# Kernel tuning notes

Hardware: AMD Instinct MI355X
Metric: run time of the kernel (lower is better)

Reference implementation:

```python
import jax, jax.numpy as jnp
import numpy as np

N_NODES = 100000
N_EDGES = 1000000
D_IN = 64
D_OUT = 64


def setup_inputs() -> dict:
    key = jax.random.key(0)
    k_x, k_e, k_w, k_b = jax.random.split(key, 4)
    x = jax.random.normal(k_x, (N_NODES, D_IN), dtype=jnp.float32)
    edge_index = jax.random.randint(k_e, (2, N_EDGES), 0, N_NODES, dtype=jnp.int64)
    # degrees of destination nodes (what the caller is expected to supply);
    # clamp to >=1 to avoid division by zero for isolated nodes
    deg = jax.ops.segment_sum(jnp.ones((N_EDGES,), jnp.float32), edge_index[1], num_segments=N_NODES)
    node_degrees = jnp.maximum(deg, 1.0)
    W = jax.random.normal(k_w, (D_OUT, D_IN), dtype=jnp.float32) * (1.0 / np.sqrt(D_IN))
    b = jax.random.normal(k_b, (D_OUT,), dtype=jnp.float32) * 0.01
    return {"x": x, "edge_index": edge_index, "node_degrees": node_degrees, "W": W, "b": b}


def reference(x, edge_index, node_degrees, W, b):
    # Original does argsort+cumsum+boundary segment-sum; mathematically this is
    # a scatter-add of gathered neighbor features into dst, i.e. a segment sum.
    src, dst = edge_index[0], edge_index[1]
    agg = jax.ops.segment_sum(x[src], dst, num_segments=x.shape[0])  # [N, D_IN]
    mean = agg / node_degrees[:, None]
    return mean @ W.T + b  # [N, D_OUT]
```

## Files before the change

### kernel.cpp

```cpp
#include <hip/hip_runtime.h>


#define D 64
#define BSHIFT 7
#define BNODES (1 << BSHIFT)
#define CAP 2048
#define GTHREADS 512
#define PERTHREAD (CAP / GTHREADS)
#define MAXB 2048

__device__ inline int detect_stride_block(const unsigned* __restrict__ words,
                                          int E, int* sflag) {
    int t = threadIdx.x;
    if (t < 64) {
        unsigned v = (t < E) ? words[2 * t + 1] : 0u;
        int any = __any(v != 0u);
        if (t == 0) *sflag = any ? 1 : 2;
    }
    __syncthreads();
    return *sflag;
}

__device__ inline unsigned pack_bf16(float a, float b) {
    unsigned ua = __float_as_uint(a), ub = __float_as_uint(b);
    ua += 0x7fffu + ((ua >> 16) & 1u);
    ub += 0x7fffu + ((ub >> 16) & 1u);
    return (ua >> 16) | (ub & 0xffff0000u);
}

__global__ __launch_bounds__(256) void deg_bucket_hist(
        const float* __restrict__ deg, int* __restrict__ bcnt, int N, int nb) {
    __shared__ int lh[8];
    int t = threadIdx.x;
    if (t < 8) lh[t] = 0;
    __syncthreads();
    int n0 = blockIdx.x * 1024 + t * 4;
    int v = 0;
    #pragma unroll
    for (int j = 0; j < 4; ++j) { int n = n0 + j; if (n < N) v += (int)(deg[n] + 0.5f); }
    atomicAdd(&lh[t >> 5], v);
    __syncthreads();
    if (t < 8) {
        int b = blockIdx.x * 8 + t;
        if (b < nb) bcnt[b] = lh[t];
    }
}

__global__ __launch_bounds__(256) void bucket_scan(
        const int* __restrict__ bcnt, int* __restrict__ offs,
        int* __restrict__ cursor, int nb) {
    __shared__ int s[256];
    int t = threadIdx.x;
    int c[8]; int v = 0;
    #pragma unroll
    for (int j = 0; j < 8; ++j) {
        int i = t * 8 + j;
        c[j] = (i < nb) ? bcnt[i] : 0;
        v += c[j];
    }
    int own = v;
    s[t] = v;
    __syncthreads();
    for (int off = 1; off < 256; off <<= 1) {
        int u = (t >= off) ? s[t - off] : 0;
        __syncthreads();
        s[t] += u;
        __syncthreads();
    }
    int run = s[t] - own;
    #pragma unroll
    for (int j = 0; j < 8; ++j) {
        int i = t * 8 + j;
        if (i < nb) { offs[i] = run; cursor[i] = run; run += c[j]; }
    }
}

__global__ __launch_bounds__(256) void partition_kernel(
        const unsigned* __restrict__ ewords, int* __restrict__ cursor,
        unsigned* __restrict__ pairs, int E, int nb) {
    __shared__ int sflag;
    __shared__ int lhist[MAXB];
    __shared__ int lbase[MAXB];
    int s = detect_stride_block(ewords, E, &sflag);
    int t = threadIdx.x;
    for (int sub = 0; sub < 2; ++sub) {
        int base = blockIdx.x * 8192 + sub * 4096;
        if (base >= E) break;
        for (int i = t; i < nb; i += 256) lhist[i] = 0;
        __syncthreads();
        unsigned pv[16]; int bk[16];
        #pragma unroll
        for (int k = 0; k < 16; ++k) {
            int e = base + k * 256 + t;
            bk[k] = -1;
            if (e < E) {
                unsigned src = ewords[(size_t)e * s];
                unsigned dst = ewords[((size_t)E + e) * s];
                bk[k] = (int)(dst >> BSHIFT);
                pv[k] = src | ((dst & (BNODES - 1)) << 17);
                atomicAdd(&lhist[bk[k]], 1);
            }
        }
        __syncthreads();
        for (int hb = t; hb < nb; hb += 256) {
            int cc = lhist[hb];
            if (cc) lbase[hb] = atomicAdd(&cursor[hb], cc);
            lhist[hb] = 0;
        }
        __syncthreads();
        #pragma unroll
        for (int k = 0; k < 16; ++k) {
            if (bk[k] >= 0) {
                int lpos = atomicAdd(&lhist[bk[k]], 1);
                pairs[lbase[bk[k]] + lpos] = pv[k];
            }
        }
        __syncthreads();
    }
}

__global__ __launch_bounds__(256, 4) void xw_kernel(
        const float* __restrict__ x, const float* __restrict__ W,
        unsigned* __restrict__ y2, int N) {
    __shared__ float Wt[64 * 68];
    __shared__ float xs[64 * 68];
    int t = threadIdx.x;
    for (int i = t; i < 64 * 64; i += 256) {
        int o = i >> 6, k = i & 63;
        Wt[k * 68 + o] = W[i];
    }
    int base = blockIdx.x * 64;
    int row = t >> 4, c4 = (t & 15) * 4;
    #pragma unroll
    for (int r = 0; r < 4; ++r) {
        int nl = row + r * 16;
        int n = base + nl;
        float4 v = {0.f, 0.f, 0.f, 0.f};
        if (n < N) v = *(const float4*)(x + (size_t)n * 64 + c4);
        *(float4*)&xs[nl * 68 + c4] = v;
    }
    __syncthreads();
    int o4 = (t & 15) * 4, nl4 = (t >> 4) * 4;
    float acc[4][4];
    #pragma unroll
    for (int i = 0; i < 4; ++i)
        #pragma unroll
        for (int j = 0; j < 4; ++j) acc[i][j] = 0.f;
    #pragma unroll 2
    for (int k0 = 0; k0 < 64; k0 += 4) {
        float a[4][4], wv[4][4];
        #pragma unroll
        for (int i = 0; i < 4; ++i)
            *(float4*)a[i] = *(const float4*)&xs[(nl4 + i) * 68 + k0];
        #pragma unroll
        for (int dk = 0; dk < 4; ++dk)
            *(float4*)wv[dk] = *(const float4*)&Wt[(k0 + dk) * 68 + o4];
        #pragma unroll
        for (int i = 0; i < 4; ++i)
            #pragma unroll
            for (int j = 0; j < 4; ++j)
                acc[i][j] += a[i][0] * wv[0][j] + a[i][1] * wv[1][j]
                           + a[i][2] * wv[2][j] + a[i][3] * wv[3][j];
    }
    int n0 = base + nl4;
    #pragma unroll
    for (int i = 0; i < 4; ++i) {
        if (n0 + i < N) {
            uint2 p;
            p.x = pack_bf16(acc[i][0], acc[i][1]);
            p.y = pack_bf16(acc[i][2], acc[i][3]);
            *(uint2*)(y2 + (size_t)(n0 + i) * 32 + (o4 >> 1)) = p;
        }
    }
}

__global__ __launch_bounds__(GTHREADS) void bucket_gather(
        const unsigned* __restrict__ y2, const unsigned* __restrict__ pairs,
        const int* __restrict__ offs, const int* __restrict__ endc,
        const float* __restrict__ deg, const float* __restrict__ b,
        float* __restrict__ out, int N) {
    __shared__ unsigned list[CAP];
    __shared__ int cnt[BNODES], st[BNODES], sc[BNODES];
    int t = threadIdx.x;
    int bkt = blockIdx.x, base = bkt << BSHIFT;
    int start = offs[bkt], end = endc[bkt];
    int lane = t & 63, w = t >> 6;
    int g = lane >> 4, c = lane & 15;
    float4 bv = ((const float4*)b)[c];
    int nchunk = (end - start + CAP - 1) / CAP;
    if (nchunk < 1) nchunk = 1;

    for (int ci = 0; ci < nchunk; ++ci) {
        int e0 = start + ci * CAP;
        int cn = end - e0; if (cn > CAP) cn = CAP; if (cn < 0) cn = 0;
        if (t < BNODES) cnt[t] = 0;
        __syncthreads();
        unsigned pv[PERTHREAD];
        #pragma unroll
        for (int j = 0; j < PERTHREAD; ++j) {
            int i = t + j * GTHREADS;
            pv[j] = (i < cn) ? pairs[e0 + i] : 0xFFFFFFFFu;
            if (i < cn) atomicAdd(&cnt[pv[j] >> 17], 1);
        }
        __syncthreads();
        if (t < BNODES) sc[t] = cnt[t];
        __syncthreads();
        for (int off = 1; off < BNODES; off <<= 1) {
            int v = (t < BNODES && t >= off) ? sc[t - off] : 0;
            __syncthreads();
            if (t < BNODES) sc[t] += v;
            __syncthreads();
        }
        if (t < BNODES) { st[t] = sc[t] - cnt[t]; sc[t] = sc[t] - cnt[t]; }
        __syncthreads();
        #pragma unroll
        for (int j = 0; j < PERTHREAD; ++j) {
            if (pv[j] != 0xFFFFFFFFu) {
                int pos = atomicAdd(&sc[pv[j] >> 17], 1);
                list[pos] = pv[j] & 0x1FFFFu;
            }
        }
        __syncthreads();

        for (int nl0 = w * 16; nl0 < w * 16 + 16; nl0 += 4) {
            int mynode = nl0 + g;
            int n = base + mynode;
            int s0 = st[mynode], e1 = s0 + cnt[mynode];
            float ax = 0.f, ay = 0.f, az = 0.f, aw = 0.f;
            for (int i = s0; i < e1; ++i) {
                unsigned src = list[i];
                uint2 u = *(const uint2*)(y2 + (size_t)src * 32 + c * 2);
                ax += __uint_as_float(u.x << 16);
                ay += __uint_as_float(u.x & 0xffff0000u);
                az += __uint_as_float(u.y << 16);
                aw += __uint_as_float(u.y & 0xffff0000u);
            }
            if (n < N) {
                float* op = out + (size_t)n * 64 + c * 4;
                if (nchunk == 1) {
                    float invd = 1.0f / deg[n];
                    float4 o4 = {ax * invd + bv.x, ay * invd + bv.y,
                                 az * invd + bv.z, aw * invd + bv.w};
                    *(float4*)op = o4;
                } else {
                    float4 p = {0.f, 0.f, 0.f, 0.f};
                    if (ci > 0) p = *(const float4*)op;
                    p.x += ax; p.y += ay; p.z += az; p.w += aw;
                    if (ci == nchunk - 1) {
                        float invd = 1.0f / deg[n];
                        p = {p.x * invd + bv.x, p.y * invd + bv.y,
                             p.z * invd + bv.z, p.w * invd + bv.w};
                    }
                    *(float4*)op = p;
                }
            }
        }
        __syncthreads();
    }
}

__global__ __launch_bounds__(256) void scatter_kernel(
        const float* __restrict__ x, const unsigned* __restrict__ ewords,
        float* __restrict__ agg, int E) {
    __shared__ int sflag;
    int s = detect_stride_block(ewords, E, &sflag);
    int gid = blockIdx.x * blockDim.x + threadIdx.x;
    int e = gid >> 4, q = gid & 15;
    if (e >= E) return;
    int src = (int)ewords[(size_t)e * s];
    int dst = (int)ewords[((size_t)E + e) * s];
    const float4 v = *(const float4*)(x + (size_t)src * D + q * 4);
    float* p = agg + (size_t)dst * D + q * 4;
    unsafeAtomicAdd(p + 0, v.x);
    unsafeAtomicAdd(p + 1, v.y);
    unsafeAtomicAdd(p + 2, v.z);
    unsafeAtomicAdd(p + 3, v.w);
}

__global__ __launch_bounds__(256) void gemm_kernel(
        float* __restrict__ inout, const float* __restrict__ deg,
        const float* __restrict__ W, const float* __restrict__ b, int nNodes) {
    __shared__ float Wt[64 * 65];
    __shared__ float rows[4 * 64];
    int t = threadIdx.x;
    for (int i = t; i < 64 * 64; i += 256) {
        int o = i >> 6, k = i & 63;
        Wt[k * 65 + o] = W[i];
    }
    int base = blockIdx.x * 4;
    int nl = t >> 6, o = t & 63;
    int n = base + nl;
    if (n < nNodes) {
        float invd = 1.0f / deg[n];
        rows[nl * 64 + o] = inout[(size_t)n * 64 + o] * invd;
    }
    __syncthreads();
    if (n >= nNodes) return;
    float acc = b[o];
    #pragma unroll
    for (int k = 0; k < 64; ++k)
        acc += rows[nl * 64 + k] * Wt[k * 65 + o];
    inout[(size_t)n * 64 + o] = acc;
}

extern "C" void kernel_launch(void* const* d_in, const int* in_sizes, int n_in,
                              void* d_out, int out_size, void* d_ws, size_t ws_size,
                              hipStream_t stream) {
    const float*    x      = (const float*)d_in[0];
    const unsigned* ewords = (const unsigned*)d_in[1];
    const float*    deg    = (const float*)d_in[2];
    const float*    W      = (const float*)d_in[3];
    const float*    b      = (const float*)d_in[4];
    float*          out    = (float*)d_out;

    const int E = in_sizes[1] / 2;
    const int N = in_sizes[2];
    const int nb = (N + BNODES - 1) >> BSHIFT;

    char* ws = (char*)d_ws;
    size_t bcntB = MAXB * 4, offB = MAXB * 4, curB = MAXB * 4;
    size_t pairB = (((size_t)E + N) * 4 + 63) & ~63ull;
    size_t need  = bcntB + offB + curB + pairB + (size_t)N * 32 * 4;

    if (ws_size >= need && N < (1 << 17) && nb <= MAXB) {
        int*      bcnt   = (int*)ws;
        int*      offs   = (int*)(ws + bcntB);
        int*      cursor = (int*)(ws + bcntB + offB);
        unsigned* pairs  = (unsigned*)(ws + bcntB + offB + curB);
        unsigned* y2     = (unsigned*)(ws + bcntB + offB + curB + pairB);

        deg_bucket_hist<<<(N + 1023) / 1024, 256, 0, stream>>>(deg, bcnt, N, nb);
        bucket_scan<<<1, 256, 0, stream>>>(bcnt, offs, cursor, nb);
        partition_kernel<<<(E + 8191) / 8192, 256, 0, stream>>>(
            ewords, cursor, pairs, E, nb);
        xw_kernel<<<(N + 63) / 64, 256, 0, stream>>>(x, W, y2, N);
        bucket_gather<<<nb, GTHREADS, 0, stream>>>(
            y2, pairs, offs, cursor, deg, b, out, N);
    } else {
        hipMemsetAsync(d_out, 0, (size_t)out_size * sizeof(float), stream);
        long long sthreads = (long long)E * 16;
        int sblocks = (int)((sthreads + 255) / 256);
        scatter_kernel<<<sblocks, 256, 0, stream>>>(x, ewords, out, E);
        gemm_kernel<<<(N + 3) / 4, 256, 0, stream>>>(out, deg, W, b, N);
    }
}
```

Measured before the change: 161.6 us.

## Use fixed-capacity edge buckets with spill and fuse partition with XW GEMM

```diff
diff --git a/kernel.cpp b/kernel.cpp
--- a/kernel.cpp
+++ b/kernel.cpp
@@ -28,234 +28,189 @@
     return (ua >> 16) | (ub & 0xffff0000u);
 }
 
-__global__ __launch_bounds__(256) void deg_bucket_hist(
-        const float* __restrict__ deg, int* __restrict__ bcnt, int N, int nb) {
-    __shared__ int lh[8];
+__global__ __launch_bounds__(256, 4) void partition_xw_kernel(
+        const unsigned* __restrict__ ewords, int* __restrict__ cursor,
+        unsigned* __restrict__ pairs, uint2* __restrict__ spill,
+        int* __restrict__ spillCnt,
+        const float* __restrict__ x, const float* __restrict__ W,
+        unsigned* __restrict__ y2, int E, int N, int nb, int pblocks) {
+    __shared__ __align__(16) char smem[34832];
     int t = threadIdx.x;
-    if (t < 8) lh[t] = 0;
-    __syncthreads();
-    int n0 = blockIdx.x * 1024 + t * 4;
-    int v = 0;
-    #pragma unroll
-    for (int j = 0; j < 4; ++j) { int n = n0 + j; if (n < N) v += (int)(deg[n] + 0.5f); }
-    atomicAdd(&lh[t >> 5], v);
-    __syncthreads();
-    if (t < 8) {
-        int b = blockIdx.x * 8 + t;
-        if (b < nb) bcnt[b] = lh[t];
-    }
-}
-
-__global__ __launch_bounds__(256) void bucket_scan(
-        const int* __restrict__ bcnt, int* __restrict__ offs,
-        int* __restrict__ cursor, int nb) {
-    __shared__ int s[256];
-    int t = threadIdx.x;
-    int c[8]; int v = 0;
-    #pragma unroll
-    for (int j = 0; j < 8; ++j) {
-        int i = t * 8 + j;
-        c[j] = (i < nb) ? bcnt[i] : 0;
-        v += c[j];
-    }
-    int own = v;
-    s[t] = v;
-    __syncthreads();
-    for (int off = 1; off < 256; off <<= 1) {
-        int u = (t >= off) ? s[t - off] : 0;
+
+    if ((int)blockIdx.x < pblocks) {
+        int* lhist = (int*)smem;
+        int* lbase = lhist + MAXB;
+        int* sflag = lbase + MAXB;
+        int s = detect_stride_block(ewords, E, sflag);
+        for (int sub = 0; sub < 2; ++sub) {
+            int base = blockIdx.x * 8192 + sub * 4096;
+            if (base >= E) break;
+            for (int i = t; i < nb; i += 256) lhist[i] = 0;
+            __syncthreads();
+            unsigned pv[16]; int bk[16];
+            #pragma unroll
+            for (int k = 0; k < 16; ++k) {
+                int e = base + k * 256 + t;
+                bk[k] = -1;
+                if (e < E) {
+                    unsigned src = ewords[(size_t)e * s];
+                    unsigned dst = ewords[((size_t)E + e) * s];
+                    bk[k] = (int)(dst >> BSHIFT);
+                    pv[k] = src | ((dst & (BNODES - 1)) << 17);
+                    atomicAdd(&lhist[bk[k]], 1);
+                }
+            }
+            __syncthreads();
+            for (int hb = t; hb < nb; hb += 256) {
+                int cc = lhist[hb];
+                if (cc) lbase[hb] = atomicAdd(&cursor[hb], cc);
+                lhist[hb] = 0;
+            }
+            __syncthreads();
+            #pragma unroll
+            for (int k = 0; k < 16; ++k) {
+                if (bk[k] >= 0) {
+                    int lpos = lbase[bk[k]] + atomicAdd(&lhist[bk[k]], 1);
+                    if (lpos < CAP) {
+                        pairs[(size_t)bk[k] * CAP + lpos] = pv[k];
+                    } else {
+                        int si = atomicAdd(spillCnt, 1);
+                        unsigned dst = ((unsigned)bk[k] << BSHIFT) | (pv[k] >> 17);
+                        spill[si] = make_uint2(pv[k] & 0x1FFFFu, dst);
+                    }
+                }
+            }
+            __syncthreads();
+        }
+    } else {
+        float* Wt = (float*)smem;
+        float* xs = Wt + 64 * 68;
+        for (int i = t; i < 64 * 64; i += 256) {
+            int o = i >> 6, k = i & 63;
+            Wt[k * 68 + o] = W[i];
+        }
+        int base = ((int)blockIdx.x - pblocks) * 64;
+        int row = t >> 4, c4 = (t & 15) * 4;
+        #pragma unroll
+        for (int r = 0; r < 4; ++r) {
+            int nl = row + r * 16;
+            int n = base + nl;
+            float4 v = {0.f, 0.f, 0.f, 0.f};
+            if (n < N) v = *(const float4*)(x + (size_t)n * 64 + c4);
+            *(float4*)&xs[nl * 68 + c4] = v;
+        }
         __syncthreads();
-        s[t] += u;
-        __syncthreads();
-    }
-    int run = s[t] - own;
-    #pragma unroll
-    for (int j = 0; j < 8; ++j) {
-        int i = t * 8 + j;
-        if (i < nb) { offs[i] = run; cursor[i] = run; run += c[j]; }
-    }
-}
-
-__global__ __launch_bounds__(256) void partition_kernel(
-        const unsigned* __restrict__ ewords, int* __restrict__ cursor,
-        unsigned* __restrict__ pairs, int E, int nb) {
-    __shared__ int sflag;
-    __shared__ int lhist[MAXB];
-    __shared__ int lbase[MAXB];
-    int s = detect_stride_block(ewords, E, &sflag);
-    int t = threadIdx.x;
-    for (int sub = 0; sub < 2; ++sub) {
-        int base = blockIdx.x * 8192 + sub * 4096;
-        if (base >= E) break;
-        for (int i = t; i < nb; i += 256) lhist[i] = 0;
-        __syncthreads();
-        unsigned pv[16]; int bk[16];
-        #pragma unroll
-        for (int k = 0; k < 16; ++k) {
-            int e = base + k * 256 + t;
-            bk[k] = -1;
-            if (e < E) {
-                unsigned src = ewords[(size_t)e * s];
-                unsigned dst = ewords[((size_t)E + e) * s];
-                bk[k] = (int)(dst >> BSHIFT);
-                pv[k] = src | ((dst & (BNODES - 1)) << 17);
-                atomicAdd(&lhist[bk[k]], 1);
-            }
-        }
-        __syncthreads();
-        for (int hb = t; hb < nb; hb += 256) {
-            int cc = lhist[hb];
-            if (cc) lbase[hb] = atomicAdd(&cursor[hb], cc);
-            lhist[hb] = 0;
-        }
-        __syncthreads();
-        #pragma unroll
-        for (int k = 0; k < 16; ++k) {
-            if (bk[k] >= 0) {
-                int lpos = atomicAdd(&lhist[bk[k]], 1);
-                pairs[lbase[bk[k]] + lpos] = pv[k];
-            }
-        }
-        __syncthreads();
-    }
-}
-
-__global__ __launch_bounds__(256, 4) void xw_kernel(
-        const float* __restrict__ x, const float* __restrict__ W,
-        unsigned* __restrict__ y2, int N) {
-    __shared__ float Wt[64 * 68];
-    __shared__ float xs[64 * 68];
-    int t = threadIdx.x;
-    for (int i = t; i < 64 * 64; i += 256) {
-        int o = i >> 6, k = i & 63;
-        Wt[k * 68 + o] = W[i];
-    }
-    int base = blockIdx.x * 64;
-    int row = t >> 4, c4 = (t & 15) * 4;
-    #pragma unroll
-    for (int r = 0; r < 4; ++r) {
-        int nl = row + r * 16;
-        int n = base + nl;
-        float4 v = {0.f, 0.f, 0.f, 0.f};
-        if (n < N) v = *(const float4*)(x + (size_t)n * 64 + c4);
-        *(float4*)&xs[nl * 68 + c4] = v;
-    }
-    __syncthreads();
-    int o4 = (t & 15) * 4, nl4 = (t >> 4) * 4;
-    float acc[4][4];
-    #pragma unroll
-    for (int i = 0; i < 4; ++i)
-        #pragma unroll
-        for (int j = 0; j < 4; ++j) acc[i][j] = 0.f;
-    #pragma unroll 2
-    for (int k0 = 0; k0 < 64; k0 += 4) {
-        float a[4][4], wv[4][4];
+        int o4 = (t & 15) * 4, nl4 = (t >> 4) * 4;
+        float acc[4][4];
         #pragma unroll
         for (int i = 0; i < 4; ++i)
-            *(float4*)a[i] = *(const float4*)&xs[(nl4 + i) * 68 + k0];
+            #pragma unroll
+            for (int j = 0; j < 4; ++j) acc[i][j] = 0.f;
+        #pragma unroll 2
+        for (int k0 = 0; k0 < 64; k0 += 4) {
+            float a[4][4], wv[4][4];
+            #pragma unroll
+            for (int i = 0; i < 4; ++i)
+                *(float4*)a[i] = *(const float4*)&xs[(nl4 + i) * 68 + k0];
+            #pragma unroll
+            for (int dk = 0; dk < 4; ++dk)
+                *(float4*)wv[dk] = *(const float4*)&Wt[(k0 + dk) * 68 + o4];
+            #pragma unroll
+            for (int i = 0; i < 4; ++i)
+                #pragma unroll
+                for (int j = 0; j < 4; ++j)
+                    acc[i][j] += a[i][0] * wv[0][j] + a[i][1] * wv[1][j]
+                               + a[i][2] * wv[2][j] + a[i][3] * wv[3][j];
+        }
+        int n0 = base + nl4;
         #pragma unroll
-        for (int dk = 0; dk < 4; ++dk)
-            *(float4*)wv[dk] = *(const float4*)&Wt[(k0 + dk) * 68 + o4];
-        #pragma unroll
-        for (int i = 0; i < 4; ++i)
-            #pragma unroll
-            for (int j = 0; j < 4; ++j)
-                acc[i][j] += a[i][0] * wv[0][j] + a[i][1] * wv[1][j]
-                           + a[i][2] * wv[2][j] + a[i][3] * wv[3][j];
-    }
-    int n0 = base + nl4;
-    #pragma unroll
-    for (int i = 0; i < 4; ++i) {
-        if (n0 + i < N) {
-            uint2 p;
-            p.x = pack_bf16(acc[i][0], acc[i][1]);
-            p.y = pack_bf16(acc[i][2], acc[i][3]);
-            *(uint2*)(y2 + (size_t)(n0 + i) * 32 + (o4 >> 1)) = p;
+        for (int i = 0; i < 4; ++i) {
+            if (n0 + i < N) {
+                uint2 p;
+                p.x = pack_bf16(acc[i][0], acc[i][1]);
+                p.y = pack_bf16(acc[i][2], acc[i][3]);
+                *(uint2*)(y2 + (size_t)(n0 + i) * 32 + (o4 >> 1)) = p;
+            }
         }
     }
 }
 
 __global__ __launch_bounds__(GTHREADS) void bucket_gather(
         const unsigned* __restrict__ y2, const unsigned* __restrict__ pairs,
-        const int* __restrict__ offs, const int* __restrict__ endc,
+        const int* __restrict__ cursor, const uint2* __restrict__ spill,
+        const int* __restrict__ spillCnt,
         const float* __restrict__ deg, const float* __restrict__ b,
         float* __restrict__ out, int N) {
     __shared__ unsigned list[CAP];
     __shared__ int cnt[BNODES], st[BNODES], sc[BNODES];
     int t = threadIdx.x;
     int bkt = blockIdx.x, base = bkt << BSHIFT;
-    int start = offs[bkt], end = endc[bkt];
+    int total = cursor[bkt];
+    int cn = total < CAP ? total : CAP;
     int lane = t & 63, w = t >> 6;
     int g = lane >> 4, c = lane & 15;
     float4 bv = ((const float4*)b)[c];
-    int nchunk = (end - start + CAP - 1) / CAP;
-    if (nchunk < 1) nchunk = 1;
-
-    for (int ci = 0; ci < nchunk; ++ci) {
-        int e0 = start + ci * CAP;
-        int cn = end - e0; if (cn > CAP) cn = CAP; if (cn < 0) cn = 0;
-        if (t < BNODES) cnt[t] = 0;
+
+    if (t < BNODES) cnt[t] = 0;
+    __syncthreads();
+    unsigned pv[PERTHREAD];
+    #pragma unroll
+    for (int j = 0; j < PERTHREAD; ++j) {
+        int i = t + j * GTHREADS;
+        pv[j] = (i < cn) ? pairs[(size_t)bkt * CAP + i] : 0xFFFFFFFFu;
+        if (i < cn) atomicAdd(&cnt[pv[j] >> 17], 1);
+    }
+    __syncthreads();
+    if (t < BNODES) sc[t] = cnt[t];
+    __syncthreads();
+    for (int off = 1; off < BNODES; off <<= 1) {
+        int v = (t < BNODES && t >= off) ? sc[t - off] : 0;
         __syncthreads();
-        unsigned pv[PERTHREAD];
-        #pragma unroll
-        for (int j = 0; j < PERTHREAD; ++j) {
-            int i = t + j * GTHREADS;
-            pv[j] = (i < cn) ? pairs[e0 + i] : 0xFFFFFFFFu;
-            if (i < cn) atomicAdd(&cnt[pv[j] >> 17], 1);
-        }
+        if (t < BNODES) sc[t] += v;
         __syncthreads();
-        if (t < BNODES) sc[t] = cnt[t];
-        __syncthreads();
-        for (int off = 1; off < BNODES; off <<= 1) {
-            int v = (t < BNODES && t >= off) ? sc[t - off] : 0;
-            __syncthreads();
-            if (t < BNODES) sc[t] += v;
-            __syncthreads();
-        }
-        if (t < BNODES) { st[t] = sc[t] - cnt[t]; sc[t] = sc[t] - cnt[t]; }
-        __syncthreads();
-        #pragma unroll
-        for (int j = 0; j < PERTHREAD; ++j) {
-            if (pv[j] != 0xFFFFFFFFu) {
-                int pos = atomicAdd(&sc[pv[j] >> 17], 1);
-                list[pos] = pv[j] & 0x1FFFFu;
-            }
-        }
-        __syncthreads();
-
-        for (int nl0 = w * 16; nl0 < w * 16 + 16; nl0 += 4) {
-            int mynode = nl0 + g;
-            int n = base + mynode;
-            int s0 = st[mynode], e1 = s0 + cnt[mynode];
-            float ax = 0.f, ay = 0.f, az = 0.f, aw = 0.f;
-            for (int i = s0; i < e1; ++i) {
-                unsigned src = list[i];
-                uint2 u = *(const uint2*)(y2 + (size_t)src * 32 + c * 2);
+    }
+    if (t < BNODES) { st[t] = sc[t] - cnt[t]; sc[t] = sc[t] - cnt[t]; }
+    __syncthreads();
+    #pragma unroll
+    for (int j = 0; j < PERTHREAD; ++j) {
+        if (pv[j] != 0xFFFFFFFFu) {
+            int pos = atomicAdd(&sc[pv[j] >> 17], 1);
+            list[pos] = pv[j] & 0x1FFFFu;
+        }
+    }
+    __syncthreads();
+
+    int scnt = *spillCnt;
+
+    for (int nl0 = w * 16; nl0 < w * 16 + 16; nl0 += 4) {
+        int mynode = nl0 + g;
+        int n = base + mynode;
+        int s0 = st[mynode], e1 = s0 + cnt[mynode];
+        float ax = 0.f, ay = 0.f, az = 0.f, aw = 0.f;
+        for (int i = s0; i < e1; ++i) {
+            unsigned src = list[i];
+            uint2 u = *(const uint2*)(y2 + (size_t)src * 32 + c * 2);
+            ax += __uint_as_float(u.x << 16);
+            ay += __uint_as_float(u.x & 0xffff0000u);
+            az += __uint_as_float(u.y << 16);
+            aw += __uint_as_float(u.y & 0xffff0000u);
+        }
+        for (int i = 0; i < scnt; ++i) {
+            uint2 e = spill[i];
+            if ((int)e.y == n) {
+                uint2 u = *(const uint2*)(y2 + (size_t)e.x * 32 + c * 2);
                 ax += __uint_as_float(u.x << 16);
                 ay += __uint_as_float(u.x & 0xffff0000u);
                 az += __uint_as_float(u.y << 16);
                 aw += __uint_as_float(u.y & 0xffff0000u);
             }
-            if (n < N) {
-                float* op = out + (size_t)n * 64 + c * 4;
-                if (nchunk == 1) {
-                    float invd = 1.0f / deg[n];
-                    float4 o4 = {ax * invd + bv.x, ay * invd + bv.y,
-                                 az * invd + bv.z, aw * invd + bv.w};
-                    *(float4*)op = o4;
-                } else {
-                    float4 p = {0.f, 0.f, 0.f, 0.f};
-                    if (ci > 0) p = *(const float4*)op;
-                    p.x += ax; p.y += ay; p.z += az; p.w += aw;
-                    if (ci == nchunk - 1) {
-                        float invd = 1.0f / deg[n];
-                        p = {p.x * invd + bv.x, p.y * invd + bv.y,
-                             p.z * invd + bv.z, p.w * invd + bv.w};
-                    }
-                    *(float4*)op = p;
-                }
-            }
-        }
-        __syncthreads();
+        }
+        if (n < N) {
+            float invd = 1.0f / deg[n];
+            float4 o4 = {ax * invd + bv.x, ay * invd + bv.y,
+                         az * invd + bv.z, aw * invd + bv.w};
+            *(float4*)(out + (size_t)n * 64 + c * 4) = o4;
+        }
     }
 }
 
@@ -318,24 +273,27 @@
     const int nb = (N + BNODES - 1) >> BSHIFT;
 
     char* ws = (char*)d_ws;
-    size_t bcntB = MAXB * 4, offB = MAXB * 4, curB = MAXB * 4;
-    size_t pairB = (((size_t)E + N) * 4 + 63) & ~63ull;
-    size_t need  = bcntB + offB + curB + pairB + (size_t)N * 32 * 4;
+    size_t curB  = (MAXB + 16) * 4;
+    size_t pairB = ((size_t)nb * CAP * 4 + 63) & ~63ull;
+    size_t spB   = ((size_t)E * 8 + 63) & ~63ull;
+    size_t need  = curB + pairB + spB + (size_t)N * 32 * 4;
 
     if (ws_size >= need && N < (1 << 17) && nb <= MAXB) {
-        int*      bcnt   = (int*)ws;
-        int*      offs   = (int*)(ws + bcntB);
-        int*      cursor = (int*)(ws + bcntB + offB);
-        unsigned* pairs  = (unsigned*)(ws + bcntB + offB + curB);
-        unsigned* y2     = (unsigned*)(ws + bcntB + offB + curB + pairB);
-
-        deg_bucket_hist<<<(N + 1023) / 1024, 256, 0, stream>>>(deg, bcnt, N, nb);
-        bucket_scan<<<1, 256, 0, stream>>>(bcnt, offs, cursor, nb);
-        partition_kernel<<<(E + 8191) / 8192, 256, 0, stream>>>(
-            ewords, cursor, pairs, E, nb);
-        xw_kernel<<<(N + 63) / 64, 256, 0, stream>>>(x, W, y2, N);
+        int*      cursor   = (int*)ws;
+        int*      spillCnt = cursor + MAXB;
+        unsigned* pairs    = (unsigned*)(ws + curB);
+        uint2*    spill    = (uint2*)(ws + curB + pairB);
+        unsigned* y2       = (unsigned*)(ws + curB + pairB + spB);
+
+        hipMemsetAsync(cursor, 0, curB, stream);
+
+        int pblocks  = (E + 8191) / 8192;
+        int xwblocks = (N + 63) / 64;
+        partition_xw_kernel<<<pblocks + xwblocks, 256, 0, stream>>>(
+            ewords, cursor, pairs, spill, spillCnt, x, W, y2, E, N, nb, pblocks);
+
         bucket_gather<<<nb, GTHREADS, 0, stream>>>(
-            y2, pairs, offs, cursor, deg, b, out, N);
+            y2, pairs, cursor, spill, spillCnt, deg, b, out, N);
     } else {
         hipMemsetAsync(d_out, 0, (size_t)out_size * sizeof(float), stream);
         long long sthreads = (long long)E * 16;
```

Result: faster. 147.5 us (-8.8%).
